# Performance work log

Measured on AMD Instinct MI355X. Metric: run time of the kernel, lower is better.

Reference implementation:

```python
import jax, jax.numpy as jnp
import numpy as np

N, D = 2048, 64
H, W = 128, 128
NEAR, RADIUS_CLIP, BLUR = 0.01, 3.0, 0.3
A_MIN, A_MAX = 1.0 / 255.0, 0.999


def setup_inputs():
    key = jax.random.key(0)
    k = jax.random.split(key, 6)
    xy = jax.random.uniform(k[0], (N, 2), minval=-1.2, maxval=1.2)
    zz = jax.random.uniform(k[1], (N, 1), minval=3.0, maxval=5.0)
    means = jnp.concatenate([xy, zz], axis=1).astype(jnp.float32)
    quats = jax.random.normal(k[2], (N, 4), dtype=jnp.float32)
    scales = jax.random.normal(k[3], (N, 3), dtype=jnp.float32) * 0.3 - 2.2  # log-scales
    opacities = jax.random.normal(k[4], (N,), dtype=jnp.float32) * 0.5 + 1.0  # logits
    gs_features = jax.random.normal(k[5], (N, D), dtype=jnp.float32) * 0.5
    c2o = jnp.eye(4, dtype=jnp.float32)
    K = jnp.array([[200.0, 0.0, 64.0], [0.0, 200.0, 64.0], [0.0, 0.0, 1.0]], dtype=jnp.float32)
    return dict(means=means, quats=quats, scales=scales, opacities=opacities,
                gs_features=gs_features, c2o=c2o, K=K, width=W, height=H)


def _quat_to_rot(q):
    q = q / jnp.linalg.norm(q, axis=-1, keepdims=True)
    w, x, y, z = q[:, 0], q[:, 1], q[:, 2], q[:, 3]
    r0 = jnp.stack([1 - 2 * (y * y + z * z), 2 * (x * y - w * z), 2 * (x * z + w * y)], -1)
    r1 = jnp.stack([2 * (x * y + w * z), 1 - 2 * (x * x + z * z), 2 * (y * z - w * x)], -1)
    r2 = jnp.stack([2 * (x * z - w * y), 2 * (y * z + w * x), 1 - 2 * (x * x + y * y)], -1)
    return jnp.stack([r0, r1, r2], -2)  # [N,3,3]


def _rasterize(means, quats, log_scales, opac_logits, colors, viewmat, K, width, height):
    Rv, tv = viewmat[:3, :3], viewmat[:3, 3]
    fx, fy, cx, cy = K[0, 0], K[1, 1], K[0, 2], K[1, 2]
    mc = means @ Rv.T + tv                      # camera-space means [N,3]
    x, y, z = mc[:, 0], mc[:, 1], mc[:, 2]
    # 3D covariance Sigma = R S S^T R^T, rotated into camera frame
    M = _quat_to_rot(quats) * jnp.exp(log_scales)[:, None, :]
    cov_w = M @ jnp.swapaxes(M, 1, 2)           # [N,3,3]
    cov_c = jnp.einsum('ij,njk,lk->nil', Rv, cov_w, Rv)
    # perspective (EWA) Jacobian [N,2,3]
    rz = 1.0 / z
    zero = jnp.zeros_like(z)
    J = jnp.stack([jnp.stack([fx * rz, zero, -fx * x * rz * rz], -1),
                   jnp.stack([zero, fy * rz, -fy * y * rz * rz], -1)], -2)
    cov2d = jnp.einsum('nij,njk,nlk->nil', J, cov_c, J)
    a = cov2d[:, 0, 0] + BLUR
    b = cov2d[:, 0, 1]
    c = cov2d[:, 1, 1] + BLUR
    det = a * c - b * b
    cA, cB, cC = c / det, -b / det, a / det     # conic = inverse 2D covariance
    mx = fx * x * rz + cx
    my = fy * y * rz + cy
    # cull: behind near plane, degenerate, or projected 3-sigma radius below radius_clip
    lam_max = 0.5 * (a + c) + jnp.sqrt(jnp.maximum(0.25 * (a - c) ** 2 + b * b, 1e-12))
    radius = 3.0 * jnp.sqrt(lam_max)
    valid = (z > NEAR) & (det > 0) & (radius > RADIUS_CLIP)
    opac = jax.nn.sigmoid(opac_logits)
    # global front-to-back depth order (single camera)
    order = jnp.argsort(z)
    mx, my, cA, cB, cC = mx[order], my[order], cA[order], cB[order], cC[order]
    opac, valid, colors = opac[order], valid[order], colors[order]
    # per pixel-gaussian evaluation, [H,W,N]
    px = jnp.arange(width, dtype=means.dtype) + 0.5
    py = jnp.arange(height, dtype=means.dtype) + 0.5
    dx = px[None, :, None] - mx[None, None, :]
    dy = py[:, None, None] - my[None, None, :]
    sigma = 0.5 * (cA * dx * dx + cC * dy * dy) + cB * dx * dy
    alpha = jnp.minimum(opac * jnp.exp(-sigma), A_MAX)
    alpha = jnp.where((sigma >= 0) & valid & (alpha >= A_MIN), alpha, 0.0)
    # front-to-back alpha compositing: exclusive transmittance cumprod
    Tcum = jnp.cumprod(1.0 - alpha, axis=-1)
    T_excl = jnp.concatenate([jnp.ones_like(Tcum[..., :1]), Tcum[..., :-1]], axis=-1)
    out = jnp.einsum('hwn,nd->hwd', alpha * T_excl, colors)
    return out[None]  # [1,H,W,D]


def reference(means, quats, scales, opacities, gs_features, c2o, K, width, height):
    viewmat = jnp.linalg.inv(c2o)
    return _rasterize(means, quats, scales, opacities, gs_features, viewmat, K, width, height)
```

## Files before the change

### kernel.cpp

```cpp
#include <hip/hip_runtime.h>

constexpr int NG  = 2048;
constexpr int DF  = 64;
constexpr int IW  = 128;
constexpr int IH  = 128;
constexpr int NZ  = 8;
constexpr int RB  = 1024;
constexpr int CAP = 1024;
constexpr int NBK = 256;

#define P_NEAR 0.01f
#define P_BLUR 0.3f
#define P_AMIN (1.0f/255.0f)
#define P_AMAX 0.999f

constexpr int L_T    = 0;
constexpr int L_CNT  = 512;
constexpr int L_SIDX = 528;
constexpr int L_OVL  = L_SIDX + CAP;
constexpr int L_PRM  = L_OVL;
constexpr int L_KEYS = L_PRM + CAP * 8;
constexpr int L_KS2  = L_KEYS + CAP * 2;
constexpr int L_HIST = L_KS2 + CAP * 2;
constexpr int L_STRT = L_HIST + NBK;
constexpr int L_CURS = L_STRT + NBK;
constexpr int L_SCN  = L_CURS + NBK;
constexpr int L_ACC  = L_OVL;
constexpr int ACC_ST = 66;
constexpr int L_TOTAL = L_OVL + NZ * 64 * ACC_ST;

__device__ inline void invert4x4(const float* m, float* inv) {
    inv[0]  =  m[5]*m[10]*m[15] - m[5]*m[11]*m[14] - m[9]*m[6]*m[15] + m[9]*m[7]*m[14] + m[13]*m[6]*m[11] - m[13]*m[7]*m[10];
    inv[4]  = -m[4]*m[10]*m[15] + m[4]*m[11]*m[14] + m[8]*m[6]*m[15] - m[8]*m[7]*m[14] - m[12]*m[6]*m[11] + m[12]*m[7]*m[10];
    inv[8]  =  m[4]*m[9]*m[15]  - m[4]*m[11]*m[13] - m[8]*m[5]*m[15] + m[8]*m[7]*m[13] + m[12]*m[5]*m[11] - m[12]*m[7]*m[9];
    inv[12] = -m[4]*m[9]*m[14]  + m[4]*m[10]*m[13] + m[8]*m[5]*m[14] - m[8]*m[6]*m[13] - m[12]*m[5]*m[10] + m[12]*m[6]*m[9];
    inv[1]  = -m[1]*m[10]*m[15] + m[1]*m[11]*m[14] + m[9]*m[2]*m[15] - m[9]*m[3]*m[14] - m[13]*m[2]*m[11] + m[13]*m[3]*m[10];
    inv[5]  =  m[0]*m[10]*m[15] - m[0]*m[11]*m[14] - m[8]*m[2]*m[15] + m[8]*m[3]*m[14] + m[12]*m[2]*m[11] - m[12]*m[3]*m[10];
    inv[9]  = -m[0]*m[9]*m[15]  + m[0]*m[11]*m[13] + m[8]*m[1]*m[15] - m[8]*m[3]*m[13] - m[12]*m[1]*m[11] + m[12]*m[3]*m[9];
    inv[13] =  m[0]*m[9]*m[14]  - m[0]*m[10]*m[13] - m[8]*m[1]*m[14] + m[8]*m[2]*m[13] + m[12]*m[1]*m[10] - m[12]*m[2]*m[9];
    inv[2]  =  m[1]*m[6]*m[15]  - m[1]*m[7]*m[14]  - m[5]*m[2]*m[15] + m[5]*m[3]*m[14] + m[13]*m[2]*m[7]  - m[13]*m[3]*m[6];
    inv[6]  = -m[0]*m[6]*m[15]  + m[0]*m[7]*m[14]  + m[4]*m[2]*m[15] - m[4]*m[3]*m[14] - m[12]*m[2]*m[7]  + m[12]*m[3]*m[6];
    inv[10] =  m[0]*m[5]*m[15]  - m[0]*m[7]*m[13]  - m[4]*m[1]*m[15] + m[4]*m[3]*m[13] + m[12]*m[1]*m[7]  - m[12]*m[3]*m[5];
    inv[14] = -m[0]*m[5]*m[14]  + m[0]*m[6]*m[13]  + m[4]*m[1]*m[14] - m[4]*m[2]*m[13] - m[12]*m[1]*m[6]  + m[12]*m[2]*m[5];
    inv[3]  = -m[1]*m[6]*m[11]  + m[1]*m[7]*m[10]  + m[5]*m[2]*m[11] - m[5]*m[3]*m[10] - m[9]*m[2]*m[7]   + m[9]*m[3]*m[6];
    inv[7]  =  m[0]*m[6]*m[11]  - m[0]*m[7]*m[10]  - m[4]*m[2]*m[11] + m[4]*m[3]*m[10] + m[8]*m[2]*m[7]   - m[8]*m[3]*m[6];
    inv[11] = -m[0]*m[5]*m[11]  + m[0]*m[7]*m[9]   + m[4]*m[1]*m[11] - m[4]*m[3]*m[9]  - m[8]*m[1]*m[7]   + m[8]*m[3]*m[5];
    inv[15] =  m[0]*m[5]*m[10]  - m[0]*m[6]*m[9]   - m[4]*m[1]*m[10] + m[4]*m[2]*m[9]  + m[8]*m[1]*m[6]   - m[8]*m[2]*m[5];
    float det = m[0]*inv[0] + m[1]*inv[4] + m[2]*inv[8] + m[3]*inv[12];
    det = 1.0f / det;
    #pragma unroll
    for (int i = 0; i < 16; ++i) inv[i] *= det;
}

__global__ __launch_bounds__(RB, 4) void fused_render_kernel(
    const float* __restrict__ means,  const float* __restrict__ quats,
    const float* __restrict__ scales, const float* __restrict__ opac_logits,
    const float* __restrict__ colors, const float* __restrict__ c2o,
    const float* __restrict__ Kmat,   float* __restrict__ out)
{
    extern __shared__ float lds[];
    int*                cnt  = (int*)(lds + L_CNT);
    int*                sidx = (int*)(lds + L_SIDX);
    unsigned long long* keys = (unsigned long long*)(lds + L_KEYS);
    unsigned long long* ks2  = (unsigned long long*)(lds + L_KS2);
    int*                hist = (int*)(lds + L_HIST);
    int*                strt = (int*)(lds + L_STRT);
    int*                curs = (int*)(lds + L_CURS);
    int*                scn  = (int*)(lds + L_SCN);
    float4*             prm4 = (float4*)(lds + L_PRM);

    const int tid  = threadIdx.x;
    const int lane = tid & 63;
    const int wv16 = tid >> 6;
    const int sz   = wv16 >> 1;
    const int hh   = wv16 & 1;
    const int tile = blockIdx.x;
    const int tx = (tile & 15) * 8;
    const int ty = (tile >> 4) * 8;
    const float px = tx + (lane & 7) + 0.5f;
    const float py = ty + (lane >> 3) + 0.5f;
    const float cxt = tx + 4.0f, cyt = ty + 4.0f;

    if (tid == 0) *cnt = 0;
    __syncthreads();

    {
        float inv[16];
        {
            float m[16];
            #pragma unroll
            for (int t = 0; t < 16; ++t) m[t] = c2o[t];
            invert4x4(m, inv);
        }
        const float fx = Kmat[0], fy = Kmat[4], cx = Kmat[2], cy = Kmat[5];

        #pragma unroll
        for (int c = 0; c < NG / RB; ++c) {
            const int g = c * RB + tid;
            float mx = means[g*3+0], my = means[g*3+1], mz = means[g*3+2];
            float X = inv[0]*mx + inv[1]*my + inv[2]*mz  + inv[3];
            float Y = inv[4]*mx + inv[5]*my + inv[6]*mz  + inv[7];
            float Z = inv[8]*mx + inv[9]*my + inv[10]*mz + inv[11];

            float qw = quats[g*4+0], qx = quats[g*4+1], qy = quats[g*4+2], qz = quats[g*4+3];
            float qn = rsqrtf(qw*qw + qx*qx + qy*qy + qz*qz);
            qw *= qn; qx *= qn; qy *= qn; qz *= qn;
            float R00 = 1.f - 2.f*(qy*qy + qz*qz), R01 = 2.f*(qx*qy - qw*qz), R02 = 2.f*(qx*qz + qw*qy);
            float R10 = 2.f*(qx*qy + qw*qz), R11 = 1.f - 2.f*(qx*qx + qz*qz), R12 = 2.f*(qy*qz - qw*qx);
            float R20 = 2.f*(qx*qz - qw*qy), R21 = 2.f*(qy*qz + qw*qx), R22 = 1.f - 2.f*(qx*qx + qy*qy);

            float s0 = expf(scales[g*3+0]), s1 = expf(scales[g*3+1]), s2 = expf(scales[g*3+2]);
            float M00 = R00*s0, M01 = R01*s1, M02 = R02*s2;
            float M10 = R10*s0, M11 = R11*s1, M12 = R12*s2;
            float M20 = R20*s0, M21 = R21*s1, M22 = R22*s2;

            float V00 = M00*M00 + M01*M01 + M02*M02;
            float V01 = M00*M10 + M01*M11 + M02*M12;
            float V02 = M00*M20 + M01*M21 + M02*M22;
            float V11 = M10*M10 + M11*M11 + M12*M12;
            float V12 = M10*M20 + M11*M21 + M12*M22;
            float V22 = M20*M20 + M21*M21 + M22*M22;

            float Rv[3][3] = {{inv[0],inv[1],inv[2]},{inv[4],inv[5],inv[6]},{inv[8],inv[9],inv[10]}};
            float Vm[3][3] = {{V00,V01,V02},{V01,V11,V12},{V02,V12,V22}};
            float Tm[3][3], C[3][3];
            #pragma unroll
            for (int r = 0; r < 3; ++r)
                #pragma unroll
                for (int cc = 0; cc < 3; ++cc)
                    Tm[r][cc] = Rv[r][0]*Vm[0][cc] + Rv[r][1]*Vm[1][cc] + Rv[r][2]*Vm[2][cc];
            #pragma unroll
            for (int r = 0; r < 3; ++r)
                #pragma unroll
                for (int cc = 0; cc < 3; ++cc)
                    C[r][cc] = Tm[r][0]*Rv[cc][0] + Tm[r][1]*Rv[cc][1] + Tm[r][2]*Rv[cc][2];

            float rz = 1.0f / Z;
            float j00 = fx*rz, j02 = -fx*X*rz*rz;
            float j11 = fy*rz, j12 = -fy*Y*rz*rz;

            float c00 = j00*j00*C[0][0] + 2.f*j00*j02*C[0][2] + j02*j02*C[2][2];
            float c01 = j00*j11*C[0][1] + j00*j12*C[0][2] + j02*j11*C[1][2] + j02*j12*C[2][2];
            float c11 = j11*j11*C[1][1] + 2.f*j11*j12*C[1][2] + j12*j12*C[2][2];

            float a = c00 + P_BLUR;
            float b = c01;
            float cc_ = c11 + P_BLUR;
            float det = a*cc_ - b*b;

            float pmx = fx*X*rz + cx;
            float pmy = fy*Y*rz + cy;

            float lam = 0.5f*(a + cc_) + sqrtf(fmaxf(0.25f*(a - cc_)*(a - cc_) + b*b, 1e-12f));
            float radius = 3.0f * sqrtf(lam);
            bool valid = (Z > P_NEAR) && (det > 0.0f) && (radius > 3.0f);

            float op = 1.0f / (1.0f + expf(-opac_logits[g]));

            bool sel = false;
            float cA = 0.f, cB = 0.f, cC2 = 0.f;
            if (valid) {
                float rdet = 1.0f / det;
                cA = cc_ * rdet; cB = -b * rdet; cC2 = a * rdet;
                float smax = logf(255.0f * op);
                if (smax > 0.f) {
                    float rx = sqrtf(2.f * a   * smax) * 1.0001f + 1e-3f;
                    float ry = sqrtf(2.f * cc_ * smax) * 1.0001f + 1e-3f;
                    sel = (fabsf(pmx - cxt) <= rx + 3.5f) && (fabsf(pmy - cyt) <= ry + 3.5f);
                }
            }

            unsigned long long m = __ballot(sel);
            int wbase = 0;
            if (lane == 0 && m) wbase = atomicAdd(cnt, (int)__popcll(m));
            wbase = __shfl(wbase, 0);
            if (sel) {
                int pos = wbase + (int)__popcll(m & ((1ull << lane) - 1ull));
                if (pos < CAP) {
                    prm4[pos*2]   = make_float4(pmx, pmy, cA, cB);
                    prm4[pos*2+1] = make_float4(cC2, op, __int_as_float(g), 0.f);
                    keys[pos] = ((unsigned long long)__float_as_uint(Z) << 32) | (unsigned)g;
                }
            }
        }
    }
    __syncthreads();
    int L = *cnt;
    if (L > CAP) L = CAP;

    {
        float zl = 1e30f, zh = -1e30f;
        if (tid < L) {
            float z = __uint_as_float((unsigned)(keys[tid] >> 32));
            zl = z; zh = z;
        }
        #pragma unroll
        for (int o = 32; o; o >>= 1) {
            zl = fminf(zl, __shfl_down(zl, o));
            zh = fmaxf(zh, __shfl_down(zh, o));
        }
        if (lane == 0) { lds[L_SCN + wv16] = zl; lds[L_SCN + 16 + wv16] = zh; }
    }
    __syncthreads();
    if (tid == 0) {
        float a = lds[L_SCN], b = lds[L_SCN + 16];
        for (int i = 1; i < 16; ++i) {
            a = fminf(a, lds[L_SCN + i]); b = fmaxf(b, lds[L_SCN + 16 + i]);
        }
        lds[L_SCN + 32] = a; lds[L_SCN + 33] = b;
    }
    __syncthreads();
    const float zmin = lds[L_SCN + 32];
    const float zmax = lds[L_SCN + 33];
    const float binv = (zmax > zmin) ? ((float)NBK / (zmax - zmin)) * 0.999999f : 0.f;
    __syncthreads();

    if (tid < NBK) { hist[tid] = 0; curs[tid] = 0; }
    __syncthreads();
    int myb = 0; unsigned long long myk = 0;
    if (tid < L) {
        myk = keys[tid];
        float z = __uint_as_float((unsigned)(myk >> 32));
        myb = (int)((z - zmin) * binv);
        myb = max(0, min(myb, NBK - 1));
        atomicAdd(&hist[myb], 1);
    }
    __syncthreads();

    if (tid < NBK) scn[tid] = hist[tid];
    __syncthreads();
    for (int o = 1; o < NBK; o <<= 1) {
        int t = (tid < NBK && tid >= o) ? scn[tid - o] : 0;
        __syncthreads();
        if (tid < NBK) scn[tid] += t;
        __syncthreads();
    }
    if (tid < NBK) strt[tid] = scn[tid] - hist[tid];
    __syncthreads();

    if (tid < L) {
        int pos = strt[myb] + atomicAdd(&curs[myb], 1);
        ks2[pos]  = myk;
        sidx[pos] = tid;
    }
    __syncthreads();

    if (tid < NBK) {
        int s = strt[tid], e = s + hist[tid];
        for (int i = s + 1; i < e; ++i) {
            unsigned long long k = ks2[i]; int sl = sidx[i];
            int j = i - 1;
            while (j >= s && ks2[j] > k) {
                ks2[j+1] = ks2[j]; sidx[j+1] = sidx[j]; --j;
            }
            ks2[j+1] = k; sidx[j+1] = sl;
        }
    }
    __syncthreads();

    float acc[32];
    #pragma unroll
    for (int f = 0; f < 32; ++f) acc[f] = 0.f;
    float T = 1.0f;

    {
        const int r0 = (sz * L) >> 3;
        const int r1 = ((sz + 1) * L) >> 3;
        const float4* cph = (const float4*)colors + hh * 8;
        if (r1 > r0) {
            int k = sidx[r0];
            float4 e0 = prm4[k*2], e1 = prm4[k*2+1];
            for (int r = r0; r < r1; ++r) {
                int kn = (r + 1 < r1) ? sidx[r + 1] : k;
                float4 n0 = prm4[kn*2], n1 = prm4[kn*2+1];

                float dx = px - e0.x, dy = py - e0.y;
                float sig = 0.5f*(e0.z*dx*dx + e1.x*dy*dy) + e0.w*dx*dy;
                float al = fminf(e1.y * __expf(-sig), P_AMAX);
                al = (sig >= 0.f && al >= P_AMIN) ? al : 0.f;

                if (__ballot(al > 0.f)) {
                    float wv = T * al;
                    const float4* crow = cph + (size_t)(unsigned)__float_as_int(e1.z) * 16;
                    #pragma unroll
                    for (int q = 0; q < 8; ++q) {
                        float4 cv = crow[q];
                        acc[4*q+0] = fmaf(wv, cv.x, acc[4*q+0]);
                        acc[4*q+1] = fmaf(wv, cv.y, acc[4*q+1]);
                        acc[4*q+2] = fmaf(wv, cv.z, acc[4*q+2]);
                        acc[4*q+3] = fmaf(wv, cv.w, acc[4*q+3]);
                    }
                    T *= (1.f - al);
                    if (!__ballot(T >= 1e-6f)) break;
                }
                e0 = n0; e1 = n1; k = kn;
            }
        }
    }

    if (hh == 0) lds[L_T + sz*64 + lane] = T;
    __syncthreads();
    {
        float* ab = lds + L_ACC + (size_t)(sz * 64 + lane) * ACC_ST + hh * 32;
        #pragma unroll
        for (int q = 0; q < 16; ++q)
            *(float2*)(ab + 2*q) = make_float2(acc[2*q], acc[2*q+1]);
    }
    __syncthreads();

    {
        int p  = tid >> 4;
        int f0 = (tid & 15) * 4;
        float r0, r1, r2, r3;
        const float* ab = lds + L_ACC + (size_t)((NZ-1)*64 + p) * ACC_ST + f0;
        { float2 u = *(const float2*)ab, v = *(const float2*)(ab + 2);
          r0 = u.x; r1 = u.y; r2 = v.x; r3 = v.y; }
        #pragma unroll
        for (int s = NZ - 2; s >= 0; --s) {
            float Ts = lds[L_T + s*64 + p];
            const float* as_ = lds + L_ACC + (size_t)(s*64 + p) * ACC_ST + f0;
            float2 u = *(const float2*)as_, v = *(const float2*)(as_ + 2);
            r0 = fmaf(Ts, r0, u.x); r1 = fmaf(Ts, r1, u.y);
            r2 = fmaf(Ts, r2, v.x); r3 = fmaf(Ts, r3, v.y);
        }
        int pyg = ty + (p >> 3), pxg = tx + (p & 7);
        float* op_ = out + (size_t)(pyg * IW + pxg) * DF + f0;
        *(float4*)op_ = make_float4(r0, r1, r2, r3);
    }
}

extern "C" void kernel_launch(void* const* d_in, const int* in_sizes, int n_in,
                              void* d_out, int out_size, void* d_ws, size_t ws_size,
                              hipStream_t stream) {
    const float* means  = (const float*)d_in[0];
    const float* quats  = (const float*)d_in[1];
    const float* scales = (const float*)d_in[2];
    const float* opac   = (const float*)d_in[3];
    const float* colors = (const float*)d_in[4];
    const float* c2o    = (const float*)d_in[5];
    const float* Kmat   = (const float*)d_in[6];
    float* out = (float*)d_out;
    (void)d_ws; (void)ws_size;

    (void)hipFuncSetAttribute((const void*)fused_render_kernel,
                              hipFuncAttributeMaxDynamicSharedMemorySize,
                              L_TOTAL * 4);

    fused_render_kernel<<<IH*IW/64, RB, L_TOTAL*4, stream>>>(
        means, quats, scales, opac, colors, c2o, Kmat, out);
}
```

Measured before the change: 115.5 us.

## Split feature halves across blocks and use sixteen depth slices per tile

Each block now handles one half of the 64 feature channels for its 8x8 tile, and the launch grid doubles to 512 blocks. Within a block, all 16 waves become depth slices instead of 8 slices times 2 feature halves. The final cross-slice compositing runs in two passes of 16 channels through a smaller LDS buffer to keep shared-memory use bounded. This raises block count and depth parallelism, at the cost of every block redoing projection, binning and sorting for its tile, which doubles that per-tile setup work.

New measurement: 306.0 us. 165% more time.

```diff
diff --git a/kernel.cpp b/kernel.cpp
--- a/kernel.cpp
+++ b/kernel.cpp
@@ -4,7 +4,7 @@
 constexpr int DF  = 64;
 constexpr int IW  = 128;
 constexpr int IH  = 128;
-constexpr int NZ  = 8;
+constexpr int NZ  = 16;
 constexpr int RB  = 1024;
 constexpr int CAP = 1024;
 constexpr int NBK = 256;
@@ -15,8 +15,8 @@
 #define P_AMAX 0.999f
 
 constexpr int L_T    = 0;
-constexpr int L_CNT  = 512;
-constexpr int L_SIDX = 528;
+constexpr int L_CNT  = 1024;
+constexpr int L_SIDX = 1040;
 constexpr int L_OVL  = L_SIDX + CAP;
 constexpr int L_PRM  = L_OVL;
 constexpr int L_KEYS = L_PRM + CAP * 8;
@@ -26,7 +26,7 @@
 constexpr int L_CURS = L_STRT + NBK;
 constexpr int L_SCN  = L_CURS + NBK;
 constexpr int L_ACC  = L_OVL;
-constexpr int ACC_ST = 66;
+constexpr int ACC_ST = 17;
 constexpr int L_TOTAL = L_OVL + NZ * 64 * ACC_ST;
 
 __device__ inline void invert4x4(const float* m, float* inv) {
@@ -52,7 +52,7 @@
     for (int i = 0; i < 16; ++i) inv[i] *= det;
 }
 
-__global__ __launch_bounds__(RB, 4) void fused_render_kernel(
+__global__ __launch_bounds__(RB, 8) void fused_render_kernel(
     const float* __restrict__ means,  const float* __restrict__ quats,
     const float* __restrict__ scales, const float* __restrict__ opac_logits,
     const float* __restrict__ colors, const float* __restrict__ c2o,
@@ -71,10 +71,9 @@
 
     const int tid  = threadIdx.x;
     const int lane = tid & 63;
-    const int wv16 = tid >> 6;
-    const int sz   = wv16 >> 1;
-    const int hh   = wv16 & 1;
-    const int tile = blockIdx.x;
+    const int sz   = tid >> 6;
+    const int tile = blockIdx.x >> 1;
+    const int hh   = blockIdx.x & 1;
     const int tx = (tile & 15) * 8;
     const int ty = (tile >> 4) * 8;
     const float px = tx + (lane & 7) + 0.5f;
@@ -199,7 +198,7 @@
             zl = fminf(zl, __shfl_down(zl, o));
             zh = fmaxf(zh, __shfl_down(zh, o));
         }
-        if (lane == 0) { lds[L_SCN + wv16] = zl; lds[L_SCN + 16 + wv16] = zh; }
+        if (lane == 0) { lds[L_SCN + sz] = zl; lds[L_SCN + 16 + sz] = zh; }
     }
     __syncthreads();
     if (tid == 0) {
@@ -264,8 +263,8 @@
     float T = 1.0f;
 
     {
-        const int r0 = (sz * L) >> 3;
-        const int r1 = ((sz + 1) * L) >> 3;
+        const int r0 = (sz * L) >> 4;
+        const int r1 = ((sz + 1) * L) >> 4;
         const float4* cph = (const float4*)colors + hh * 8;
         if (r1 > r0) {
             int k = sidx[r0];
@@ -298,34 +297,32 @@
         }
     }
 
-    if (hh == 0) lds[L_T + sz*64 + lane] = T;
-    __syncthreads();
-    {
-        float* ab = lds + L_ACC + (size_t)(sz * 64 + lane) * ACC_ST + hh * 32;
-        #pragma unroll
-        for (int q = 0; q < 16; ++q)
-            *(float2*)(ab + 2*q) = make_float2(acc[2*q], acc[2*q+1]);
-    }
-    __syncthreads();
-
-    {
-        int p  = tid >> 4;
-        int f0 = (tid & 15) * 4;
-        float r0, r1, r2, r3;
-        const float* ab = lds + L_ACC + (size_t)((NZ-1)*64 + p) * ACC_ST + f0;
-        { float2 u = *(const float2*)ab, v = *(const float2*)(ab + 2);
-          r0 = u.x; r1 = u.y; r2 = v.x; r3 = v.y; }
-        #pragma unroll
-        for (int s = NZ - 2; s >= 0; --s) {
-            float Ts = lds[L_T + s*64 + p];
-            const float* as_ = lds + L_ACC + (size_t)(s*64 + p) * ACC_ST + f0;
-            float2 u = *(const float2*)as_, v = *(const float2*)(as_ + 2);
-            r0 = fmaf(Ts, r0, u.x); r1 = fmaf(Ts, r1, u.y);
-            r2 = fmaf(Ts, r2, v.x); r3 = fmaf(Ts, r3, v.y);
-        }
-        int pyg = ty + (p >> 3), pxg = tx + (p & 7);
-        float* op_ = out + (size_t)(pyg * IW + pxg) * DF + f0;
-        *(float4*)op_ = make_float4(r0, r1, r2, r3);
+    lds[L_T + sz*64 + lane] = T;
+    __syncthreads();
+
+    const int p_  = tid >> 4;
+    const int f_  = tid & 15;
+    const int pyg = ty + (p_ >> 3), pxg = tx + (p_ & 7);
+    float* opix = out + (size_t)(pyg * IW + pxg) * DF + hh*32 + f_;
+
+    #pragma unroll
+    for (int c = 0; c < 2; ++c) {
+        if (c) __syncthreads();
+        {
+            float* ab = lds + L_ACC + (size_t)(sz * 64 + lane) * ACC_ST;
+            #pragma unroll
+            for (int q = 0; q < 16; ++q) ab[q] = acc[c*16 + q];
+        }
+        __syncthreads();
+        {
+            float r = lds[L_ACC + (size_t)((NZ-1)*64 + p_) * ACC_ST + f_];
+            #pragma unroll
+            for (int s = NZ - 2; s >= 0; --s) {
+                float Ts = lds[L_T + s*64 + p_];
+                r = fmaf(Ts, r, lds[L_ACC + (size_t)(s*64 + p_) * ACC_ST + f_]);
+            }
+            opix[c*16] = r;
+        }
     }
 }
 
@@ -346,6 +343,6 @@
                               hipFuncAttributeMaxDynamicSharedMemorySize,
                               L_TOTAL * 4);
 
-    fused_render_kernel<<<IH*IW/64, RB, L_TOTAL*4, stream>>>(
+    fused_render_kernel<<<IH*IW/64 * 2, RB, L_TOTAL*4, stream>>>(
         means, quats, scales, opac, colors, c2o, Kmat, out);
 }
```

## Split fused renderer into prep/sort, per-slice render, and combine kernels via workspace

Applied to the files above, without the earlier changes.

Adds a three-kernel path used when the workspace is large enough. The first kernel does per-tile preprocessing and depth sorting and writes sorted parameters to global memory. The second renders each depth slice in its own small 128-thread block, so there are 2048 blocks instead of 256 large ones. The third composites the slices per tile. This targets the poor occupancy and load imbalance of the single 1024-thread fused kernel, at the cost of global-memory round trips and two extra launches. The old fused kernel is kept as a fallback.

Result: slower. 126.5 us (+9.5%).

```diff
diff --git a/kernel.cpp b/kernel.cpp
--- a/kernel.cpp
+++ b/kernel.cpp
@@ -4,30 +4,49 @@
 constexpr int DF  = 64;
 constexpr int IW  = 128;
 constexpr int IH  = 128;
-constexpr int NZ  = 8;
-constexpr int RB  = 1024;
 constexpr int CAP = 1024;
 constexpr int NBK = 256;
+constexpr int NSL = 8;
 
 #define P_NEAR 0.01f
 #define P_BLUR 0.3f
 #define P_AMIN (1.0f/255.0f)
 #define P_AMAX 0.999f
 
-constexpr int L_T    = 0;
-constexpr int L_CNT  = 512;
-constexpr int L_SIDX = 528;
-constexpr int L_OVL  = L_SIDX + CAP;
-constexpr int L_PRM  = L_OVL;
-constexpr int L_KEYS = L_PRM + CAP * 8;
-constexpr int L_KS2  = L_KEYS + CAP * 2;
-constexpr int L_HIST = L_KS2 + CAP * 2;
-constexpr int L_STRT = L_HIST + NBK;
-constexpr int L_CURS = L_STRT + NBK;
-constexpr int L_SCN  = L_CURS + NBK;
-constexpr int L_ACC  = L_OVL;
-constexpr int ACC_ST = 66;
-constexpr int L_TOTAL = L_OVL + NZ * 64 * ACC_ST;
+constexpr size_t W_CNT = 0;
+constexpr size_t W_PRM = 256;
+constexpr size_t W_T   = W_PRM + 256ull*CAP*8;
+constexpr size_t W_ACC = W_T   + 256ull*NSL*64;
+constexpr size_t W_END = W_ACC + 256ull*NSL*2*32*64;
+constexpr size_t WS_NEED = W_END * 4;
+
+constexpr int A_CNT  = 0;
+constexpr int A_SIDX = 16;
+constexpr int A_PRM  = 1040;
+constexpr int A_KEYS = 9232;
+constexpr int A_KS2  = 11280;
+constexpr int A_HIST = 13328;
+constexpr int A_STRT = 13584;
+constexpr int A_CURS = 13840;
+constexpr int A_SCN  = 14096;
+constexpr int A_TOT  = 14352;
+
+constexpr int F_NZ   = 8;
+constexpr int F_RB   = 1024;
+constexpr int F_T    = 0;
+constexpr int F_CNT  = 512;
+constexpr int F_SIDX = 528;
+constexpr int F_OVL  = 1552;
+constexpr int F_PRM  = F_OVL;
+constexpr int F_KEYS = F_PRM + CAP*8;
+constexpr int F_KS2  = F_KEYS + CAP*2;
+constexpr int F_HIST = F_KS2 + CAP*2;
+constexpr int F_STRT = F_HIST + NBK;
+constexpr int F_CURS = F_STRT + NBK;
+constexpr int F_SCN  = F_CURS + NBK;
+constexpr int F_ACC  = F_OVL;
+constexpr int F_ACCST= 66;
+constexpr int F_TOT  = F_OVL + F_NZ*64*F_ACCST;
 
 __device__ inline void invert4x4(const float* m, float* inv) {
     inv[0]  =  m[5]*m[10]*m[15] - m[5]*m[11]*m[14] - m[9]*m[6]*m[15] + m[9]*m[7]*m[14] + m[13]*m[6]*m[11] - m[13]*m[7]*m[10];
@@ -52,22 +71,333 @@
     for (int i = 0; i < 16; ++i) inv[i] *= det;
 }
 
-__global__ __launch_bounds__(RB, 4) void fused_render_kernel(
+__device__ inline bool preprocess_one(
+    int g, const float* __restrict__ means, const float* __restrict__ quats,
+    const float* __restrict__ scales, const float* __restrict__ opac_logits,
+    const float* inv, float fx, float fy, float cx, float cy,
+    float cxt, float cyt,
+    float4& p0, float4& p1, unsigned long long& key)
+{
+    float mx = means[g*3+0], my = means[g*3+1], mz = means[g*3+2];
+    float X = inv[0]*mx + inv[1]*my + inv[2]*mz  + inv[3];
+    float Y = inv[4]*mx + inv[5]*my + inv[6]*mz  + inv[7];
+    float Z = inv[8]*mx + inv[9]*my + inv[10]*mz + inv[11];
+
+    float qw = quats[g*4+0], qx = quats[g*4+1], qy = quats[g*4+2], qz = quats[g*4+3];
+    float qn = rsqrtf(qw*qw + qx*qx + qy*qy + qz*qz);
+    qw *= qn; qx *= qn; qy *= qn; qz *= qn;
+    float R00 = 1.f - 2.f*(qy*qy + qz*qz), R01 = 2.f*(qx*qy - qw*qz), R02 = 2.f*(qx*qz + qw*qy);
+    float R10 = 2.f*(qx*qy + qw*qz), R11 = 1.f - 2.f*(qx*qx + qz*qz), R12 = 2.f*(qy*qz - qw*qx);
+    float R20 = 2.f*(qx*qz - qw*qy), R21 = 2.f*(qy*qz + qw*qx), R22 = 1.f - 2.f*(qx*qx + qy*qy);
+
+    float s0 = expf(scales[g*3+0]), s1 = expf(scales[g*3+1]), s2 = expf(scales[g*3+2]);
+    float M00 = R00*s0, M01 = R01*s1, M02 = R02*s2;
+    float M10 = R10*s0, M11 = R11*s1, M12 = R12*s2;
+    float M20 = R20*s0, M21 = R21*s1, M22 = R22*s2;
+
+    float V00 = M00*M00 + M01*M01 + M02*M02;
+    float V01 = M00*M10 + M01*M11 + M02*M12;
+    float V02 = M00*M20 + M01*M21 + M02*M22;
+    float V11 = M10*M10 + M11*M11 + M12*M12;
+    float V12 = M10*M20 + M11*M21 + M12*M22;
+    float V22 = M20*M20 + M21*M21 + M22*M22;
+
+    float Rv[3][3] = {{inv[0],inv[1],inv[2]},{inv[4],inv[5],inv[6]},{inv[8],inv[9],inv[10]}};
+    float Vm[3][3] = {{V00,V01,V02},{V01,V11,V12},{V02,V12,V22}};
+    float Tm[3][3], C[3][3];
+    #pragma unroll
+    for (int r = 0; r < 3; ++r)
+        #pragma unroll
+        for (int cc = 0; cc < 3; ++cc)
+            Tm[r][cc] = Rv[r][0]*Vm[0][cc] + Rv[r][1]*Vm[1][cc] + Rv[r][2]*Vm[2][cc];
+    #pragma unroll
+    for (int r = 0; r < 3; ++r)
+        #pragma unroll
+        for (int cc = 0; cc < 3; ++cc)
+            C[r][cc] = Tm[r][0]*Rv[cc][0] + Tm[r][1]*Rv[cc][1] + Tm[r][2]*Rv[cc][2];
+
+    float rz = 1.0f / Z;
+    float j00 = fx*rz, j02 = -fx*X*rz*rz;
+    float j11 = fy*rz, j12 = -fy*Y*rz*rz;
+
+    float c00 = j00*j00*C[0][0] + 2.f*j00*j02*C[0][2] + j02*j02*C[2][2];
+    float c01 = j00*j11*C[0][1] + j00*j12*C[0][2] + j02*j11*C[1][2] + j02*j12*C[2][2];
+    float c11 = j11*j11*C[1][1] + 2.f*j11*j12*C[1][2] + j12*j12*C[2][2];
+
+    float a = c00 + P_BLUR;
+    float b = c01;
+    float cc_ = c11 + P_BLUR;
+    float det = a*cc_ - b*b;
+
+    float pmx = fx*X*rz + cx;
+    float pmy = fy*Y*rz + cy;
+
+    float lam = 0.5f*(a + cc_) + sqrtf(fmaxf(0.25f*(a - cc_)*(a - cc_) + b*b, 1e-12f));
+    float radius = 3.0f * sqrtf(lam);
+    bool valid = (Z > P_NEAR) && (det > 0.0f) && (radius > 3.0f);
+
+    float op = 1.0f / (1.0f + expf(-opac_logits[g]));
+
+    bool sel = false;
+    float cA = 0.f, cB = 0.f, cC2 = 0.f;
+    if (valid) {
+        float rdet = 1.0f / det;
+        cA = cc_ * rdet; cB = -b * rdet; cC2 = a * rdet;
+        float smax = logf(255.0f * op);
+        if (smax > 0.f) {
+            float rx = sqrtf(2.f * a   * smax) * 1.0001f + 1e-3f;
+            float ry = sqrtf(2.f * cc_ * smax) * 1.0001f + 1e-3f;
+            sel = (fabsf(pmx - cxt) <= rx + 3.5f) && (fabsf(pmy - cyt) <= ry + 3.5f);
+        }
+    }
+    p0 = make_float4(pmx, pmy, cA, cB);
+    p1 = make_float4(cC2, op, __int_as_float(g), 0.f);
+    key = ((unsigned long long)__float_as_uint(Z) << 32) | (unsigned)g;
+    return sel;
+}
+
+__global__ __launch_bounds__(1024) void prep_sort_tile_kernel(
+    const float* __restrict__ means,  const float* __restrict__ quats,
+    const float* __restrict__ scales, const float* __restrict__ opac_logits,
+    const float* __restrict__ c2o,    const float* __restrict__ Kmat,
+    float* __restrict__ ws)
+{
+    extern __shared__ float lds[];
+    int*                cnt  = (int*)(lds + A_CNT);
+    int*                sidx = (int*)(lds + A_SIDX);
+    unsigned long long* keys = (unsigned long long*)(lds + A_KEYS);
+    unsigned long long* ks2  = (unsigned long long*)(lds + A_KS2);
+    int*                hist = (int*)(lds + A_HIST);
+    int*                strt = (int*)(lds + A_STRT);
+    int*                curs = (int*)(lds + A_CURS);
+    int*                scn  = (int*)(lds + A_SCN);
+    float4*             prm4 = (float4*)(lds + A_PRM);
+
+    const int tid  = threadIdx.x;
+    const int lane = tid & 63;
+    const int wv   = tid >> 6;
+    const int tile = blockIdx.x;
+    const float cxt = (tile & 15) * 8 + 4.0f;
+    const float cyt = (tile >> 4) * 8 + 4.0f;
+
+    if (tid == 0) *cnt = 0;
+    __syncthreads();
+
+    float inv[16];
+    {
+        float m[16];
+        #pragma unroll
+        for (int t = 0; t < 16; ++t) m[t] = c2o[t];
+        invert4x4(m, inv);
+    }
+    const float fx = Kmat[0], fy = Kmat[4], cx = Kmat[2], cy = Kmat[5];
+
+    #pragma unroll
+    for (int c = 0; c < NG / 1024; ++c) {
+        const int g = c * 1024 + tid;
+        float4 p0, p1; unsigned long long key;
+        bool sel = preprocess_one(g, means, quats, scales, opac_logits,
+                                  inv, fx, fy, cx, cy, cxt, cyt, p0, p1, key);
+        unsigned long long m = __ballot(sel);
+        int wbase = 0;
+        if (lane == 0 && m) wbase = atomicAdd(cnt, (int)__popcll(m));
+        wbase = __shfl(wbase, 0);
+        if (sel) {
+            int pos = wbase + (int)__popcll(m & ((1ull << lane) - 1ull));
+            if (pos < CAP) {
+                prm4[pos*2] = p0; prm4[pos*2+1] = p1; keys[pos] = key;
+            }
+        }
+    }
+    __syncthreads();
+    int L = *cnt; if (L > CAP) L = CAP;
+
+    {
+        float zl = 1e30f, zh = -1e30f;
+        if (tid < L) { float z = __uint_as_float((unsigned)(keys[tid] >> 32)); zl = z; zh = z; }
+        #pragma unroll
+        for (int o = 32; o; o >>= 1) {
+            zl = fminf(zl, __shfl_down(zl, o));
+            zh = fmaxf(zh, __shfl_down(zh, o));
+        }
+        if (lane == 0) { lds[A_SCN + wv] = zl; lds[A_SCN + 16 + wv] = zh; }
+    }
+    __syncthreads();
+    if (tid == 0) {
+        float a = lds[A_SCN], b = lds[A_SCN + 16];
+        for (int i = 1; i < 16; ++i) {
+            a = fminf(a, lds[A_SCN + i]); b = fmaxf(b, lds[A_SCN + 16 + i]);
+        }
+        lds[A_SCN + 32] = a; lds[A_SCN + 33] = b;
+    }
+    __syncthreads();
+    const float zmin = lds[A_SCN + 32];
+    const float zmax = lds[A_SCN + 33];
+    const float binv = (zmax > zmin) ? ((float)NBK / (zmax - zmin)) * 0.999999f : 0.f;
+    __syncthreads();
+
+    if (tid < NBK) { hist[tid] = 0; curs[tid] = 0; }
+    __syncthreads();
+    int myb = 0; unsigned long long myk = 0;
+    if (tid < L) {
+        myk = keys[tid];
+        float z = __uint_as_float((unsigned)(myk >> 32));
+        myb = (int)((z - zmin) * binv);
+        myb = max(0, min(myb, NBK - 1));
+        atomicAdd(&hist[myb], 1);
+    }
+    __syncthreads();
+    if (tid < NBK) scn[tid] = hist[tid];
+    __syncthreads();
+    for (int o = 1; o < NBK; o <<= 1) {
+        int t = (tid < NBK && tid >= o) ? scn[tid - o] : 0;
+        __syncthreads();
+        if (tid < NBK) scn[tid] += t;
+        __syncthreads();
+    }
+    if (tid < NBK) strt[tid] = scn[tid] - hist[tid];
+    __syncthreads();
+    if (tid < L) {
+        int pos = strt[myb] + atomicAdd(&curs[myb], 1);
+        ks2[pos] = myk; sidx[pos] = tid;
+    }
+    __syncthreads();
+    if (tid < NBK) {
+        int s = strt[tid], e = s + hist[tid];
+        for (int i = s + 1; i < e; ++i) {
+            unsigned long long k = ks2[i]; int sl = sidx[i];
+            int j = i - 1;
+            while (j >= s && ks2[j] > k) { ks2[j+1] = ks2[j]; sidx[j+1] = sidx[j]; --j; }
+            ks2[j+1] = k; sidx[j+1] = sl;
+        }
+    }
+    __syncthreads();
+
+    float4* gp = (float4*)(ws + W_PRM + (size_t)tile * CAP * 8);
+    for (int i = tid; i < L; i += 1024) {
+        int sl = sidx[i];
+        gp[i*2]   = prm4[sl*2];
+        gp[i*2+1] = prm4[sl*2+1];
+    }
+    if (tid == 0) ((int*)ws)[tile] = L;
+}
+
+__global__ __launch_bounds__(128) void slice_render_kernel(
+    float* __restrict__ ws, const float* __restrict__ colors)
+{
+    const int tid  = threadIdx.x;
+    const int lane = tid & 63;
+    const int hh   = tid >> 6;
+    const int tile = blockIdx.x >> 3;
+    const int s    = blockIdx.x & 7;
+    const int tx = (tile & 15) * 8;
+    const int ty = (tile >> 4) * 8;
+    const float px = tx + (lane & 7) + 0.5f;
+    const float py = ty + (lane >> 3) + 0.5f;
+
+    const int L = min(((const int*)ws)[tile], CAP);
+    const float4* gp = (const float4*)(ws + W_PRM + (size_t)tile * CAP * 8);
+
+    float acc[32];
+    #pragma unroll
+    for (int f = 0; f < 32; ++f) acc[f] = 0.f;
+    float T = 1.0f;
+
+    const int r0 = (s * L) >> 3;
+    const int r1 = ((s + 1) * L) >> 3;
+    const float4* cph = (const float4*)colors + hh * 8;
+
+    if (r1 > r0) {
+        float4 e0 = gp[r0*2], e1 = gp[r0*2+1];
+        for (int r = r0; r < r1; ++r) {
+            int rn = (r + 1 < r1) ? r + 1 : r;
+            float4 n0 = gp[rn*2], n1 = gp[rn*2+1];
+
+            float dx = px - e0.x, dy = py - e0.y;
+            float sig = 0.5f*(e0.z*dx*dx + e1.x*dy*dy) + e0.w*dx*dy;
+            float al = fminf(e1.y * __expf(-sig), P_AMAX);
+            al = (sig >= 0.f && al >= P_AMIN) ? al : 0.f;
+
+            if (__ballot(al > 0.f)) {
+                float wv = T * al;
+                const float4* crow = cph + (size_t)(unsigned)__float_as_int(e1.z) * 16;
+                #pragma unroll
+                for (int q = 0; q < 8; ++q) {
+                    float4 cv = crow[q];
+                    acc[4*q+0] = fmaf(wv, cv.x, acc[4*q+0]);
+                    acc[4*q+1] = fmaf(wv, cv.y, acc[4*q+1]);
+                    acc[4*q+2] = fmaf(wv, cv.z, acc[4*q+2]);
+                    acc[4*q+3] = fmaf(wv, cv.w, acc[4*q+3]);
+                }
+                T *= (1.f - al);
+                if (!__ballot(T >= 1e-6f)) break;
+            }
+            e0 = n0; e1 = n1;
+        }
+    }
+
+    if (hh == 0) ws[W_T + ((size_t)tile * NSL + s) * 64 + lane] = T;
+    float* Ap = ws + W_ACC + ((((size_t)tile * NSL + s) * 2 + hh) * 32) * 64;
+    #pragma unroll
+    for (int f = 0; f < 32; ++f) Ap[f * 64 + lane] = acc[f];
+}
+
+__global__ __launch_bounds__(512) void combine_kernel(
+    const float* __restrict__ ws, float* __restrict__ out)
+{
+    __shared__ float st[64 * 65];
+    const int tid  = threadIdx.x;
+    const int tile = blockIdx.x;
+    const int tx = (tile & 15) * 8;
+    const int ty = (tile >> 4) * 8;
+
+    const int px = tid & 63;
+    const int fg = tid >> 6;
+
+    const float* Tp = ws + W_T + (size_t)tile * NSL * 64;
+    float Ts[NSL];
+    #pragma unroll
+    for (int s = 0; s < NSL; ++s) Ts[s] = Tp[s * 64 + px];
+
+    const float* Ap = ws + W_ACC + (size_t)tile * NSL * 2 * 32 * 64;
+    #pragma unroll
+    for (int j = 0; j < 8; ++j) {
+        int f = fg * 8 + j;
+        int half = f >> 5, fi = f & 31;
+        float r = Ap[(((size_t)(NSL-1) * 2 + half) * 32 + fi) * 64 + px];
+        #pragma unroll
+        for (int s = NSL - 2; s >= 0; --s)
+            r = fmaf(Ts[s], r, Ap[(((size_t)s * 2 + half) * 32 + fi) * 64 + px]);
+        st[px * 65 + f] = r;
+    }
+    __syncthreads();
+
+    const int f2 = tid & 63;
+    const int pb = (tid >> 6) * 8;
+    #pragma unroll
+    for (int k = 0; k < 8; ++k) {
+        int p2 = pb + k;
+        int pyg = ty + (p2 >> 3), pxg = tx + (p2 & 7);
+        out[(size_t)(pyg * IW + pxg) * DF + f2] = st[p2 * 65 + f2];
+    }
+}
+
+__global__ __launch_bounds__(F_RB, 4) void fused_render_kernel(
     const float* __restrict__ means,  const float* __restrict__ quats,
     const float* __restrict__ scales, const float* __restrict__ opac_logits,
     const float* __restrict__ colors, const float* __restrict__ c2o,
     const float* __restrict__ Kmat,   float* __restrict__ out)
 {
     extern __shared__ float lds[];
-    int*                cnt  = (int*)(lds + L_CNT);
-    int*                sidx = (int*)(lds + L_SIDX);
-    unsigned long long* keys = (unsigned long long*)(lds + L_KEYS);
-    unsigned long long* ks2  = (unsigned long long*)(lds + L_KS2);
-    int*                hist = (int*)(lds + L_HIST);
-    int*                strt = (int*)(lds + L_STRT);
-    int*                curs = (int*)(lds + L_CURS);
-    int*                scn  = (int*)(lds + L_SCN);
-    float4*             prm4 = (float4*)(lds + L_PRM);
+    int*                cnt  = (int*)(lds + F_CNT);
+    int*                sidx = (int*)(lds + F_SIDX);
+    unsigned long long* keys = (unsigned long long*)(lds + F_KEYS);
+    unsigned long long* ks2  = (unsigned long long*)(lds + F_KS2);
+    int*                hist = (int*)(lds + F_HIST);
+    int*                strt = (int*)(lds + F_STRT);
+    int*                curs = (int*)(lds + F_CURS);
+    int*                scn  = (int*)(lds + F_SCN);
+    float4*             prm4 = (float4*)(lds + F_PRM);
 
     const int tid  = threadIdx.x;
     const int lane = tid & 63;
@@ -93,125 +423,44 @@
             invert4x4(m, inv);
         }
         const float fx = Kmat[0], fy = Kmat[4], cx = Kmat[2], cy = Kmat[5];
-
-        #pragma unroll
-        for (int c = 0; c < NG / RB; ++c) {
-            const int g = c * RB + tid;
-            float mx = means[g*3+0], my = means[g*3+1], mz = means[g*3+2];
-            float X = inv[0]*mx + inv[1]*my + inv[2]*mz  + inv[3];
-            float Y = inv[4]*mx + inv[5]*my + inv[6]*mz  + inv[7];
-            float Z = inv[8]*mx + inv[9]*my + inv[10]*mz + inv[11];
-
-            float qw = quats[g*4+0], qx = quats[g*4+1], qy = quats[g*4+2], qz = quats[g*4+3];
-            float qn = rsqrtf(qw*qw + qx*qx + qy*qy + qz*qz);
-            qw *= qn; qx *= qn; qy *= qn; qz *= qn;
-            float R00 = 1.f - 2.f*(qy*qy + qz*qz), R01 = 2.f*(qx*qy - qw*qz), R02 = 2.f*(qx*qz + qw*qy);
-            float R10 = 2.f*(qx*qy + qw*qz), R11 = 1.f - 2.f*(qx*qx + qz*qz), R12 = 2.f*(qy*qz - qw*qx);
-            float R20 = 2.f*(qx*qz - qw*qy), R21 = 2.f*(qy*qz + qw*qx), R22 = 1.f - 2.f*(qx*qx + qy*qy);
-
-            float s0 = expf(scales[g*3+0]), s1 = expf(scales[g*3+1]), s2 = expf(scales[g*3+2]);
-            float M00 = R00*s0, M01 = R01*s1, M02 = R02*s2;
-            float M10 = R10*s0, M11 = R11*s1, M12 = R12*s2;
-            float M20 = R20*s0, M21 = R21*s1, M22 = R22*s2;
-
-            float V00 = M00*M00 + M01*M01 + M02*M02;
-            float V01 = M00*M10 + M01*M11 + M02*M12;
-            float V02 = M00*M20 + M01*M21 + M02*M22;
-            float V11 = M10*M10 + M11*M11 + M12*M12;
-            float V12 = M10*M20 + M11*M21 + M12*M22;
-            float V22 = M20*M20 + M21*M21 + M22*M22;
-
-            float Rv[3][3] = {{inv[0],inv[1],inv[2]},{inv[4],inv[5],inv[6]},{inv[8],inv[9],inv[10]}};
-            float Vm[3][3] = {{V00,V01,V02},{V01,V11,V12},{V02,V12,V22}};
-            float Tm[3][3], C[3][3];
-            #pragma unroll
-            for (int r = 0; r < 3; ++r)
-                #pragma unroll
-                for (int cc = 0; cc < 3; ++cc)
-                    Tm[r][cc] = Rv[r][0]*Vm[0][cc] + Rv[r][1]*Vm[1][cc] + Rv[r][2]*Vm[2][cc];
-            #pragma unroll
-            for (int r = 0; r < 3; ++r)
-                #pragma unroll
-                for (int cc = 0; cc < 3; ++cc)
-                    C[r][cc] = Tm[r][0]*Rv[cc][0] + Tm[r][1]*Rv[cc][1] + Tm[r][2]*Rv[cc][2];
-
-            float rz = 1.0f / Z;
-            float j00 = fx*rz, j02 = -fx*X*rz*rz;
-            float j11 = fy*rz, j12 = -fy*Y*rz*rz;
-
-            float c00 = j00*j00*C[0][0] + 2.f*j00*j02*C[0][2] + j02*j02*C[2][2];
-            float c01 = j00*j11*C[0][1] + j00*j12*C[0][2] + j02*j11*C[1][2] + j02*j12*C[2][2];
-            float c11 = j11*j11*C[1][1] + 2.f*j11*j12*C[1][2] + j12*j12*C[2][2];
-
-            float a = c00 + P_BLUR;
-            float b = c01;
-            float cc_ = c11 + P_BLUR;
-            float det = a*cc_ - b*b;
-
-            float pmx = fx*X*rz + cx;
-            float pmy = fy*Y*rz + cy;
-
-            float lam = 0.5f*(a + cc_) + sqrtf(fmaxf(0.25f*(a - cc_)*(a - cc_) + b*b, 1e-12f));
-            float radius = 3.0f * sqrtf(lam);
-            bool valid = (Z > P_NEAR) && (det > 0.0f) && (radius > 3.0f);
-
-            float op = 1.0f / (1.0f + expf(-opac_logits[g]));
-
-            bool sel = false;
-            float cA = 0.f, cB = 0.f, cC2 = 0.f;
-            if (valid) {
-                float rdet = 1.0f / det;
-                cA = cc_ * rdet; cB = -b * rdet; cC2 = a * rdet;
-                float smax = logf(255.0f * op);
-                if (smax > 0.f) {
-                    float rx = sqrtf(2.f * a   * smax) * 1.0001f + 1e-3f;
-                    float ry = sqrtf(2.f * cc_ * smax) * 1.0001f + 1e-3f;
-                    sel = (fabsf(pmx - cxt) <= rx + 3.5f) && (fabsf(pmy - cyt) <= ry + 3.5f);
-                }
-            }
-
+        #pragma unroll
+        for (int c = 0; c < NG / F_RB; ++c) {
+            const int g = c * F_RB + tid;
+            float4 p0, p1; unsigned long long key;
+            bool sel = preprocess_one(g, means, quats, scales, opac_logits,
+                                      inv, fx, fy, cx, cy, cxt, cyt, p0, p1, key);
             unsigned long long m = __ballot(sel);
             int wbase = 0;
             if (lane == 0 && m) wbase = atomicAdd(cnt, (int)__popcll(m));
             wbase = __shfl(wbase, 0);
             if (sel) {
                 int pos = wbase + (int)__popcll(m & ((1ull << lane) - 1ull));
-                if (pos < CAP) {
-                    prm4[pos*2]   = make_float4(pmx, pmy, cA, cB);
-                    prm4[pos*2+1] = make_float4(cC2, op, __int_as_float(g), 0.f);
-                    keys[pos] = ((unsigned long long)__float_as_uint(Z) << 32) | (unsigned)g;
-                }
+                if (pos < CAP) { prm4[pos*2] = p0; prm4[pos*2+1] = p1; keys[pos] = key; }
             }
         }
     }
     __syncthreads();
-    int L = *cnt;
-    if (L > CAP) L = CAP;
+    int L = *cnt; if (L > CAP) L = CAP;
 
     {
         float zl = 1e30f, zh = -1e30f;
-        if (tid < L) {
-            float z = __uint_as_float((unsigned)(keys[tid] >> 32));
-            zl = z; zh = z;
-        }
+        if (tid < L) { float z = __uint_as_float((unsigned)(keys[tid] >> 32)); zl = z; zh = z; }
         #pragma unroll
         for (int o = 32; o; o >>= 1) {
             zl = fminf(zl, __shfl_down(zl, o));
             zh = fmaxf(zh, __shfl_down(zh, o));
         }
-        if (lane == 0) { lds[L_SCN + wv16] = zl; lds[L_SCN + 16 + wv16] = zh; }
+        if (lane == 0) { lds[F_SCN + wv16] = zl; lds[F_SCN + 16 + wv16] = zh; }
     }
     __syncthreads();
     if (tid == 0) {
-        float a = lds[L_SCN], b = lds[L_SCN + 16];
-        for (int i = 1; i < 16; ++i) {
-            a = fminf(a, lds[L_SCN + i]); b = fmaxf(b, lds[L_SCN + 16 + i]);
-        }
-        lds[L_SCN + 32] = a; lds[L_SCN + 33] = b;
-    }
-    __syncthreads();
-    const float zmin = lds[L_SCN + 32];
-    const float zmax = lds[L_SCN + 33];
+        float a = lds[F_SCN], b = lds[F_SCN + 16];
+        for (int i = 1; i < 16; ++i) { a = fminf(a, lds[F_SCN + i]); b = fmaxf(b, lds[F_SCN + 16 + i]); }
+        lds[F_SCN + 32] = a; lds[F_SCN + 33] = b;
+    }
+    __syncthreads();
+    const float zmin = lds[F_SCN + 32];
+    const float zmax = lds[F_SCN + 33];
     const float binv = (zmax > zmin) ? ((float)NBK / (zmax - zmin)) * 0.999999f : 0.f;
     __syncthreads();
 
@@ -226,7 +475,6 @@
         atomicAdd(&hist[myb], 1);
     }
     __syncthreads();
-
     if (tid < NBK) scn[tid] = hist[tid];
     __syncthreads();
     for (int o = 1; o < NBK; o <<= 1) {
@@ -237,22 +485,17 @@
     }
     if (tid < NBK) strt[tid] = scn[tid] - hist[tid];
     __syncthreads();
-
     if (tid < L) {
         int pos = strt[myb] + atomicAdd(&curs[myb], 1);
-        ks2[pos]  = myk;
-        sidx[pos] = tid;
-    }
-    __syncthreads();
-
+        ks2[pos] = myk; sidx[pos] = tid;
+    }
+    __syncthreads();
     if (tid < NBK) {
         int s = strt[tid], e = s + hist[tid];
         for (int i = s + 1; i < e; ++i) {
             unsigned long long k = ks2[i]; int sl = sidx[i];
             int j = i - 1;
-            while (j >= s && ks2[j] > k) {
-                ks2[j+1] = ks2[j]; sidx[j+1] = sidx[j]; --j;
-            }
+            while (j >= s && ks2[j] > k) { ks2[j+1] = ks2[j]; sidx[j+1] = sidx[j]; --j; }
             ks2[j+1] = k; sidx[j+1] = sl;
         }
     }
@@ -262,7 +505,6 @@
     #pragma unroll
     for (int f = 0; f < 32; ++f) acc[f] = 0.f;
     float T = 1.0f;
-
     {
         const int r0 = (sz * L) >> 3;
         const int r1 = ((sz + 1) * L) >> 3;
@@ -273,12 +515,10 @@
             for (int r = r0; r < r1; ++r) {
                 int kn = (r + 1 < r1) ? sidx[r + 1] : k;
                 float4 n0 = prm4[kn*2], n1 = prm4[kn*2+1];
-
                 float dx = px - e0.x, dy = py - e0.y;
                 float sig = 0.5f*(e0.z*dx*dx + e1.x*dy*dy) + e0.w*dx*dy;
                 float al = fminf(e1.y * __expf(-sig), P_AMAX);
                 al = (sig >= 0.f && al >= P_AMIN) ? al : 0.f;
-
                 if (__ballot(al > 0.f)) {
                     float wv = T * al;
                     const float4* crow = cph + (size_t)(unsigned)__float_as_int(e1.z) * 16;
@@ -298,27 +538,26 @@
         }
     }
 
-    if (hh == 0) lds[L_T + sz*64 + lane] = T;
-    __syncthreads();
-    {
-        float* ab = lds + L_ACC + (size_t)(sz * 64 + lane) * ACC_ST + hh * 32;
+    if (hh == 0) lds[F_T + sz*64 + lane] = T;
+    __syncthreads();
+    {
+        float* ab = lds + F_ACC + (size_t)(sz * 64 + lane) * F_ACCST + hh * 32;
         #pragma unroll
         for (int q = 0; q < 16; ++q)
             *(float2*)(ab + 2*q) = make_float2(acc[2*q], acc[2*q+1]);
     }
     __syncthreads();
-
     {
         int p  = tid >> 4;
         int f0 = (tid & 15) * 4;
         float r0, r1, r2, r3;
-        const float* ab = lds + L_ACC + (size_t)((NZ-1)*64 + p) * ACC_ST + f0;
+        const float* ab = lds + F_ACC + (size_t)((F_NZ-1)*64 + p) * F_ACCST + f0;
         { float2 u = *(const float2*)ab, v = *(const float2*)(ab + 2);
           r0 = u.x; r1 = u.y; r2 = v.x; r3 = v.y; }
         #pragma unroll
-        for (int s = NZ - 2; s >= 0; --s) {
-            float Ts = lds[L_T + s*64 + p];
-            const float* as_ = lds + L_ACC + (size_t)(s*64 + p) * ACC_ST + f0;
+        for (int s = F_NZ - 2; s >= 0; --s) {
+            float Ts = lds[F_T + s*64 + p];
+            const float* as_ = lds + F_ACC + (size_t)(s*64 + p) * F_ACCST + f0;
             float2 u = *(const float2*)as_, v = *(const float2*)(as_ + 2);
             r0 = fmaf(Ts, r0, u.x); r1 = fmaf(Ts, r1, u.y);
             r2 = fmaf(Ts, r2, v.x); r3 = fmaf(Ts, r3, v.y);
@@ -340,12 +579,18 @@
     const float* c2o    = (const float*)d_in[5];
     const float* Kmat   = (const float*)d_in[6];
     float* out = (float*)d_out;
-    (void)d_ws; (void)ws_size;
-
-    (void)hipFuncSetAttribute((const void*)fused_render_kernel,
-                              hipFuncAttributeMaxDynamicSharedMemorySize,
-                              L_TOTAL * 4);
-
-    fused_render_kernel<<<IH*IW/64, RB, L_TOTAL*4, stream>>>(
-        means, quats, scales, opac, colors, c2o, Kmat, out);
-}
+
+    if (ws_size >= WS_NEED) {
+        float* ws = (float*)d_ws;
+        prep_sort_tile_kernel<<<IH*IW/64, 1024, A_TOT*4, stream>>>(
+            means, quats, scales, opac, c2o, Kmat, ws);
+        slice_render_kernel<<<IH*IW/64 * NSL, 128, 0, stream>>>(ws, colors);
+        combine_kernel<<<IH*IW/64, 512, 0, stream>>>(ws, out);
+    } else {
+        (void)hipFuncSetAttribute((const void*)fused_render_kernel,
+                                  hipFuncAttributeMaxDynamicSharedMemorySize,
+                                  F_TOT * 4);
+        fused_render_kernel<<<IH*IW/64, F_RB, F_TOT*4, stream>>>(
+            means, quats, scales, opac, colors, c2o, Kmat, out);
+    }
+}
```
